# Kernel optimization log

Measured on AMD Instinct MI355X. Metric: run time of the kernel, lower is better.

Reference implementation:

```python
import jax, jax.numpy as jnp
import numpy as np

EPS = 1e-6


def setup_inputs() -> dict:
    key = jax.random.key(0)
    k1, k2, k3, k4 = jax.random.split(key, 4)
    N, H, D = 262144, 256, 64  # total tokens, pc_hidden, cross_att_dim
    return {
        "yhat_embedding": jax.random.normal(k1, (N, H), dtype=jnp.float32),
        "y_embedding": jax.random.normal(k2, (N, H), dtype=jnp.float32),
        "k": jax.random.normal(k3, (H, D), dtype=jnp.float32),
        "q": jax.random.normal(k4, (H, D), dtype=jnp.float32),
        "seg_len": 64,  # uniform scope length (ragged scopes regularized)
    }


def reference(yhat_embedding, y_embedding, k, q, seg_len):
    # Project once for all tokens, then batch the per-segment attention.
    N, H = y_embedding.shape
    D = k.shape[1]
    B = N // seg_len
    yk = (y_embedding @ k).reshape(B, seg_len, D)       # y @ k per segment
    yq = (yhat_embedding @ q).reshape(B, seg_len, D)    # (q.T @ yhat.T).T
    scale = 1.0 / np.sqrt(D).astype(np.float32)
    # M[b] = (1/sqrt(D)) * (y@k) @ (yhat@q).T : [B, L, L]
    M = scale * jnp.einsum("bld,bmd->blm", yk, yq)
    attn = jax.nn.softmax(M, axis=2) + EPS               # softmax over dim=1 of [L,L]
    W = attn / attn.sum(axis=1, keepdims=True)           # column-normalize (axis=0 per segment)
    return W  # [B, L, L] stack of per-scope cross matrices
```

## Files before the change

### kernel.cpp

```cpp
#include <hip/hip_runtime.h>


#define H  256
#define D  64
#define L  64

typedef __attribute__((ext_vector_type(8))) short frag_b;
typedef __attribute__((ext_vector_type(4))) float frag_acc;

__device__ inline unsigned short f32_bf16_rne(float f) {
    unsigned u = __float_as_uint(f);
    u += 0x7FFFu + ((u >> 16) & 1u);
    return (unsigned short)(u >> 16);
}
__device__ inline float bf16_f32(unsigned short h) {
    return __uint_as_float(((unsigned)h) << 16);
}

__device__ inline int pswz(int row, int col) {
    return (row << 6) + ((((col >> 3) ^ row) & 7) << 3) + (col & 7);
}

__global__ void prep_kq(const float* __restrict__ k, const float* __restrict__ q,
                        unsigned short* __restrict__ planes) {
    int tid = blockIdx.x * 256 + threadIdx.x;
    const float* src = (tid < H * D) ? k : q;
    int base = (tid < H * D) ? 0 : 2 * H * D;
    int e = tid & (H * D - 1);
    int h = e >> 6, d = e & 63;
    float x = src[e];
    unsigned short hi = f32_bf16_rne(x);
    float rem = x - bf16_f32(hi);
    unsigned short lo = f32_bf16_rne(rem);
    int o = d * H + h;
    planes[base + o] = hi;
    planes[base + H * D + o] = lo;
}

__global__ __launch_bounds__(256, 5) void cross_attn(
        const float* __restrict__ yhat, const float* __restrict__ y,
        const unsigned short* __restrict__ planes, float* __restrict__ out) {
    __shared__ __align__(16) unsigned short s_pl[4 * L * D];

    const int b    = blockIdx.x;
    const int tid  = threadIdx.x;
    const int wave = tid >> 6;
    const int lane = tid & 63;
    const int ln   = lane & 15;
    const int kg   = lane >> 4;

    const bool isQ = (wave >= 2);
    const float* src = isQ ? yhat : y;
    const frag_b* bph = (const frag_b*)(planes + (isQ ? 2 * H * D : 0));
    const frag_b* bpl = bph + (H * D) / 8;
    const int rowbase = (wave & 1) * 32;

    const frag_acc zf = {0.f, 0.f, 0.f, 0.f};
    frag_acc acc[2][4];
    #pragma unroll
    for (int rt = 0; rt < 2; rt++)
        #pragma unroll
        for (int t = 0; t < 4; t++) acc[rt][t] = zf;

    const float* abase = src + ((size_t)b * L + rowbase + ln) * H + kg * 8;

    #pragma unroll 2
    for (int ks = 0; ks < 8; ks++) {
        const int kb = ks * 32;
        float4 v[2][2];
        #pragma unroll
        for (int rt = 0; rt < 2; rt++) {
            const float4* ap = (const float4*)(abase + (size_t)rt * 16 * H + kb);
            v[rt][0] = ap[0];
            v[rt][1] = ap[1];
        }
        frag_b ah[2], al[2];
        #pragma unroll
        for (int rt = 0; rt < 2; rt++) {
            float xs[8] = {v[rt][0].x, v[rt][0].y, v[rt][0].z, v[rt][0].w,
                           v[rt][1].x, v[rt][1].y, v[rt][1].z, v[rt][1].w};
            #pragma unroll
            for (int j = 0; j < 8; j++) {
                unsigned short hb = f32_bf16_rne(xs[j]);
                ah[rt][j] = (short)hb;
                al[rt][j] = (short)f32_bf16_rne(xs[j] - bf16_f32(hb));
            }
        }
        #pragma unroll
        for (int t = 0; t < 4; t++) {
            int n = t * 16 + ln;
            frag_b bh = bph[n * (H / 8) + ks * 4 + kg];
            frag_b bl = bpl[n * (H / 8) + ks * 4 + kg];
            #pragma unroll
            for (int rt = 0; rt < 2; rt++) {
                acc[rt][t] = __builtin_amdgcn_mfma_f32_16x16x32_bf16(ah[rt], bh, acc[rt][t], 0, 0, 0);
                acc[rt][t] = __builtin_amdgcn_mfma_f32_16x16x32_bf16(ah[rt], bl, acc[rt][t], 0, 0, 0);
                acc[rt][t] = __builtin_amdgcn_mfma_f32_16x16x32_bf16(al[rt], bh, acc[rt][t], 0, 0, 0);
            }
        }
    }

    {
        unsigned short* dstH = s_pl + (isQ ? 2 * L * D : 0);
        unsigned short* dstL = dstH + L * D;
        #pragma unroll
        for (int rt = 0; rt < 2; rt++)
            #pragma unroll
            for (int t = 0; t < 4; t++)
                #pragma unroll
                for (int i = 0; i < 4; i++) {
                    int row = rowbase + rt * 16 + kg * 4 + i;
                    int col = t * 16 + ln;
                    float x = acc[rt][t][i];
                    unsigned short hb = f32_bf16_rne(x);
                    int o = pswz(row, col);
                    dstH[o] = hb;
                    dstL[o] = f32_bf16_rne(x - bf16_f32(hb));
                }
    }
    __syncthreads();

    const unsigned short* ykH = s_pl;
    const unsigned short* ykL = s_pl + L * D;
    const unsigned short* yqH = s_pl + 2 * L * D;
    const unsigned short* yqL = s_pl + 3 * L * D;

    frag_acc mac[4];
    #pragma unroll
    for (int t = 0; t < 4; t++) mac[t] = zf;

    #pragma unroll
    for (int dk = 0; dk < 2; dk++) {
        const int colb = dk * 32 + kg * 8;
        frag_b ah = *(const frag_b*)(ykH + pswz(wave * 16 + ln, colb));
        frag_b al = *(const frag_b*)(ykL + pswz(wave * 16 + ln, colb));
        #pragma unroll
        for (int t = 0; t < 4; t++) {
            frag_b bh = *(const frag_b*)(yqH + pswz(t * 16 + ln, colb));
            frag_b bl = *(const frag_b*)(yqL + pswz(t * 16 + ln, colb));
            mac[t] = __builtin_amdgcn_mfma_f32_16x16x32_bf16(ah, bh, mac[t], 0, 0, 0);
            mac[t] = __builtin_amdgcn_mfma_f32_16x16x32_bf16(ah, bl, mac[t], 0, 0, 0);
            mac[t] = __builtin_amdgcn_mfma_f32_16x16x32_bf16(al, bh, mac[t], 0, 0, 0);
        }
    }
    __syncthreads();

    float* s_cs = (float*)s_pl;

    float a[4][4];
    float colpart[4] = {0.f, 0.f, 0.f, 0.f};
    #pragma unroll
    for (int i = 0; i < 4; i++) {
        float v0 = 0.125f * mac[0][i], v1 = 0.125f * mac[1][i];
        float v2 = 0.125f * mac[2][i], v3 = 0.125f * mac[3][i];
        float mx = fmaxf(fmaxf(v0, v1), fmaxf(v2, v3));
        #pragma unroll
        for (int off = 8; off >= 1; off >>= 1) mx = fmaxf(mx, __shfl_xor(mx, off, 64));
        float e0 = __expf(v0 - mx), e1 = __expf(v1 - mx);
        float e2 = __expf(v2 - mx), e3 = __expf(v3 - mx);
        float s = (e0 + e1) + (e2 + e3);
        #pragma unroll
        for (int off = 8; off >= 1; off >>= 1) s += __shfl_xor(s, off, 64);
        float rs = 1.f / s;
        a[0][i] = e0 * rs + 1e-6f; a[1][i] = e1 * rs + 1e-6f;
        a[2][i] = e2 * rs + 1e-6f; a[3][i] = e3 * rs + 1e-6f;
        colpart[0] += a[0][i]; colpart[1] += a[1][i];
        colpart[2] += a[2][i]; colpart[3] += a[3][i];
    }
    #pragma unroll
    for (int t = 0; t < 4; t++) {
        colpart[t] += __shfl_xor(colpart[t], 16, 64);
        colpart[t] += __shfl_xor(colpart[t], 32, 64);
    }
    s_cs[wave * 64 + kg * 16 + ln] = colpart[kg];
    __syncthreads();

    float* ob = out + (size_t)b * (L * L);
    #pragma unroll
    for (int t = 0; t < 4; t++) {
        int c = t * 16 + ln;
        float inv = 1.f / (s_cs[c] + s_cs[64 + c] + s_cs[128 + c] + s_cs[192 + c]);
        #pragma unroll
        for (int i = 0; i < 4; i++)
            ob[(wave * 16 + kg * 4 + i) * 64 + c] = a[t][i] * inv;
    }
}

extern "C" void kernel_launch(void* const* d_in, const int* in_sizes, int n_in,
                              void* d_out, int out_size, void* d_ws, size_t ws_size,
                              hipStream_t stream) {
    const float* yhat = (const float*)d_in[0];
    const float* y    = (const float*)d_in[1];
    const float* k    = (const float*)d_in[2];
    const float* q    = (const float*)d_in[3];
    float* outp = (float*)d_out;
    unsigned short* planes = (unsigned short*)d_ws;

    const int N = in_sizes[0] / H;
    const int B = N / L;

    prep_kq<<<(2 * H * D) / 256, 256, 0, stream>>>(k, q, planes);
    cross_attn<<<B, 256, 0, stream>>>(yhat, y, planes, outp);
}
```

Measured before the change: 604.0 us.

## Split fused cross-attention into separate projection and mixing kernels via workspace

Splits the kernel in two. A projection kernel computes y@k and yhat@q over 128-row tiles, with B fragments loaded ahead of the MFMAs, and writes swizzled bf16 hi/lo planes to the workspace. A second mixing kernel loads those planes into shared memory and runs the L×L product, softmax and column normalisation. The aim is to give the projection GEMM its own launch shape and occupancy, where before two waves per matrix did it inside a per-segment block. The cost is an extra global round trip of about 512 bytes per token. The old fused kernel stays as a fallback when the workspace is too small.

```diff
diff --git a/kernel.cpp b/kernel.cpp
--- a/kernel.cpp
+++ b/kernel.cpp
@@ -37,9 +37,88 @@
     planes[base + H * D + o] = lo;
 }
 
-__global__ __launch_bounds__(256, 5) void cross_attn(
-        const float* __restrict__ yhat, const float* __restrict__ y,
-        const unsigned short* __restrict__ planes, float* __restrict__ out) {
+__global__ __launch_bounds__(256, 4) void proj(
+        const float* __restrict__ y, const float* __restrict__ yhat,
+        const unsigned short* __restrict__ kq, unsigned short* __restrict__ pl2) {
+    const int mat  = blockIdx.y;
+    const float* src = mat ? yhat : y;
+    const frag_b* bph = (const frag_b*)(kq + mat * 2 * H * D);
+    const frag_b* bpl = bph + (H * D) / 8;
+    const int tid  = threadIdx.x;
+    const int wave = tid >> 6;
+    const int lane = tid & 63;
+    const int ln   = lane & 15;
+    const int kg   = lane >> 4;
+    const int row0 = blockIdx.x * 128 + wave * 32;
+
+    const frag_acc zf = {0.f, 0.f, 0.f, 0.f};
+    frag_acc acc[2][4];
+    #pragma unroll
+    for (int rt = 0; rt < 2; rt++)
+        #pragma unroll
+        for (int t = 0; t < 4; t++) acc[rt][t] = zf;
+
+    const float* abase = src + ((size_t)(row0 + ln)) * H + kg * 8;
+
+    #pragma unroll 2
+    for (int ks = 0; ks < 8; ks++) {
+        const int kb = ks * 32;
+        float4 v[2][2];
+        #pragma unroll
+        for (int rt = 0; rt < 2; rt++) {
+            const float4* ap = (const float4*)(abase + (size_t)rt * 16 * H + kb);
+            v[rt][0] = ap[0];
+            v[rt][1] = ap[1];
+        }
+        frag_b bh[4], bl[4];
+        #pragma unroll
+        for (int t = 0; t < 4; t++) {
+            int n = t * 16 + ln;
+            bh[t] = bph[n * (H / 8) + ks * 4 + kg];
+            bl[t] = bpl[n * (H / 8) + ks * 4 + kg];
+        }
+        frag_b ah[2], al[2];
+        #pragma unroll
+        for (int rt = 0; rt < 2; rt++) {
+            float xs[8] = {v[rt][0].x, v[rt][0].y, v[rt][0].z, v[rt][0].w,
+                           v[rt][1].x, v[rt][1].y, v[rt][1].z, v[rt][1].w};
+            #pragma unroll
+            for (int j = 0; j < 8; j++) {
+                unsigned short hb = f32_bf16_rne(xs[j]);
+                ah[rt][j] = (short)hb;
+                al[rt][j] = (short)f32_bf16_rne(xs[j] - bf16_f32(hb));
+            }
+        }
+        #pragma unroll
+        for (int t = 0; t < 4; t++)
+            #pragma unroll
+            for (int rt = 0; rt < 2; rt++) {
+                acc[rt][t] = __builtin_amdgcn_mfma_f32_16x16x32_bf16(ah[rt], bh[t], acc[rt][t], 0, 0, 0);
+                acc[rt][t] = __builtin_amdgcn_mfma_f32_16x16x32_bf16(ah[rt], bl[t], acc[rt][t], 0, 0, 0);
+                acc[rt][t] = __builtin_amdgcn_mfma_f32_16x16x32_bf16(al[rt], bh[t], acc[rt][t], 0, 0, 0);
+            }
+    }
+
+    #pragma unroll
+    for (int rt = 0; rt < 2; rt++)
+        #pragma unroll
+        for (int t = 0; t < 4; t++)
+            #pragma unroll
+            for (int i = 0; i < 4; i++) {
+                int rg  = row0 + rt * 16 + kg * 4 + i;
+                int seg = rg >> 6, r = rg & 63;
+                int col = t * 16 + ln;
+                int o   = pswz(r, col);
+                unsigned short* mb = pl2 + (size_t)seg * 16384 + mat * 8192;
+                float x = acc[rt][t][i];
+                unsigned short hb = f32_bf16_rne(x);
+                mb[o]        = hb;
+                mb[4096 + o] = f32_bf16_rne(x - bf16_f32(hb));
+            }
+}
+
+__global__ __launch_bounds__(256, 5) void mix(
+        const unsigned short* __restrict__ pl2, float* __restrict__ out) {
     __shared__ __align__(16) unsigned short s_pl[4 * L * D];
 
     const int b    = blockIdx.x;
@@ -49,6 +128,93 @@
     const int ln   = lane & 15;
     const int kg   = lane >> 4;
 
+    {
+        const float4* g4 = (const float4*)(pl2 + (size_t)b * 16384);
+        float4* s4 = (float4*)s_pl;
+        #pragma unroll
+        for (int i = 0; i < 8; i++) s4[i * 256 + tid] = g4[i * 256 + tid];
+    }
+    __syncthreads();
+
+    const unsigned short* ykH = s_pl;
+    const unsigned short* ykL = s_pl + L * D;
+    const unsigned short* yqH = s_pl + 2 * L * D;
+    const unsigned short* yqL = s_pl + 3 * L * D;
+
+    const frag_acc zf = {0.f, 0.f, 0.f, 0.f};
+    frag_acc mac[4];
+    #pragma unroll
+    for (int t = 0; t < 4; t++) mac[t] = zf;
+
+    #pragma unroll
+    for (int dk = 0; dk < 2; dk++) {
+        const int colb = dk * 32 + kg * 8;
+        frag_b ah = *(const frag_b*)(ykH + pswz(wave * 16 + ln, colb));
+        frag_b al = *(const frag_b*)(ykL + pswz(wave * 16 + ln, colb));
+        #pragma unroll
+        for (int t = 0; t < 4; t++) {
+            frag_b bh = *(const frag_b*)(yqH + pswz(t * 16 + ln, colb));
+            frag_b bl = *(const frag_b*)(yqL + pswz(t * 16 + ln, colb));
+            mac[t] = __builtin_amdgcn_mfma_f32_16x16x32_bf16(ah, bh, mac[t], 0, 0, 0);
+            mac[t] = __builtin_amdgcn_mfma_f32_16x16x32_bf16(ah, bl, mac[t], 0, 0, 0);
+            mac[t] = __builtin_amdgcn_mfma_f32_16x16x32_bf16(al, bh, mac[t], 0, 0, 0);
+        }
+    }
+    __syncthreads();
+
+    float* s_cs = (float*)s_pl;
+
+    float a[4][4];
+    float colpart[4] = {0.f, 0.f, 0.f, 0.f};
+    #pragma unroll
+    for (int i = 0; i < 4; i++) {
+        float v0 = 0.125f * mac[0][i], v1 = 0.125f * mac[1][i];
+        float v2 = 0.125f * mac[2][i], v3 = 0.125f * mac[3][i];
+        float mx = fmaxf(fmaxf(v0, v1), fmaxf(v2, v3));
+        #pragma unroll
+        for (int off = 8; off >= 1; off >>= 1) mx = fmaxf(mx, __shfl_xor(mx, off, 64));
+        float e0 = __expf(v0 - mx), e1 = __expf(v1 - mx);
+        float e2 = __expf(v2 - mx), e3 = __expf(v3 - mx);
+        float s = (e0 + e1) + (e2 + e3);
+        #pragma unroll
+        for (int off = 8; off >= 1; off >>= 1) s += __shfl_xor(s, off, 64);
+        float rs = 1.f / s;
+        a[0][i] = e0 * rs + 1e-6f; a[1][i] = e1 * rs + 1e-6f;
+        a[2][i] = e2 * rs + 1e-6f; a[3][i] = e3 * rs + 1e-6f;
+        colpart[0] += a[0][i]; colpart[1] += a[1][i];
+        colpart[2] += a[2][i]; colpart[3] += a[3][i];
+    }
+    #pragma unroll
+    for (int t = 0; t < 4; t++) {
+        colpart[t] += __shfl_xor(colpart[t], 16, 64);
+        colpart[t] += __shfl_xor(colpart[t], 32, 64);
+    }
+    s_cs[wave * 64 + kg * 16 + ln] = colpart[kg];
+    __syncthreads();
+
+    float* ob = out + (size_t)b * (L * L);
+    #pragma unroll
+    for (int t = 0; t < 4; t++) {
+        int c = t * 16 + ln;
+        float inv = 1.f / (s_cs[c] + s_cs[64 + c] + s_cs[128 + c] + s_cs[192 + c]);
+        #pragma unroll
+        for (int i = 0; i < 4; i++)
+            ob[(wave * 16 + kg * 4 + i) * 64 + c] = a[t][i] * inv;
+    }
+}
+
+__global__ __launch_bounds__(256, 5) void cross_attn_fused(
+        const float* __restrict__ yhat, const float* __restrict__ y,
+        const unsigned short* __restrict__ planes, float* __restrict__ out) {
+    __shared__ __align__(16) unsigned short s_pl[4 * L * D];
+
+    const int b    = blockIdx.x;
+    const int tid  = threadIdx.x;
+    const int wave = tid >> 6;
+    const int lane = tid & 63;
+    const int ln   = lane & 15;
+    const int kg   = lane >> 4;
+
     const bool isQ = (wave >= 2);
     const float* src = isQ ? yhat : y;
     const frag_b* bph = (const frag_b*)(planes + (isQ ? 2 * H * D : 0));
@@ -99,7 +265,6 @@
             }
         }
     }
-
     {
         unsigned short* dstH = s_pl + (isQ ? 2 * L * D : 0);
         unsigned short* dstL = dstH + L * D;
@@ -146,7 +311,6 @@
     __syncthreads();
 
     float* s_cs = (float*)s_pl;
-
     float a[4][4];
     float colpart[4] = {0.f, 0.f, 0.f, 0.f};
     #pragma unroll
@@ -200,5 +364,13 @@
     const int B = N / L;
 
     prep_kq<<<(2 * H * D) / 256, 256, 0, stream>>>(k, q, planes);
-    cross_attn<<<B, 256, 0, stream>>>(yhat, y, planes, outp);
-}
+
+    const size_t need = 128 * 1024 + (size_t)N * 512;
+    if (ws_size >= need) {
+        unsigned short* pl2 = (unsigned short*)((char*)d_ws + 128 * 1024);
+        proj<<<dim3(N / 128, 2), 256, 0, stream>>>(y, yhat, planes, pl2);
+        mix<<<B, 256, 0, stream>>>(pl2, outp);
+    } else {
+        cross_attn_fused<<<B, 256, 0, stream>>>(yhat, y, planes, outp);
+    }
+}
```

After: 650.3 us. 7.7% more time.

## Stage activation tiles through swizzled LDS with prefetch and relayout k/q fragments

Applied to the files above, without the earlier changes.

Each block now cooperatively loads the 64x256 y and yhat rows with coalesced float4 reads into a swizzled 64 KB LDS buffer. It processes two 32-row halves, prefetching the second half into registers while the first is computed. The k/q bf16 hi/lo planes are rearranged so each lane's MFMA B fragments are contiguous. This is meant to replace strided per-lane global reads with coalesced traffic, at the cost of lower occupancy (2 blocks/CU) and extra barriers.

```diff
diff --git a/kernel.cpp b/kernel.cpp
--- a/kernel.cpp
+++ b/kernel.cpp
@@ -22,25 +22,59 @@
 }
 
 __global__ void prep_kq(const float* __restrict__ k, const float* __restrict__ q,
-                        unsigned short* __restrict__ planes) {
+                        unsigned short* __restrict__ kqF) {
     int tid = blockIdx.x * 256 + threadIdx.x;
-    const float* src = (tid < H * D) ? k : q;
-    int base = (tid < H * D) ? 0 : 2 * H * D;
+    int m   = (tid >= H * D) ? 1 : 0;
+    const float* src = m ? q : k;
     int e = tid & (H * D - 1);
     int h = e >> 6, d = e & 63;
     float x = src[e];
     unsigned short hi = f32_bf16_rne(x);
-    float rem = x - bf16_f32(hi);
-    unsigned short lo = f32_bf16_rne(rem);
-    int o = d * H + h;
-    planes[base + o] = hi;
-    planes[base + H * D + o] = lo;
-}
-
-__global__ __launch_bounds__(256, 5) void cross_attn(
+    unsigned short lo = f32_bf16_rne(x - bf16_f32(hi));
+    int ks = h >> 5, kg = (h >> 3) & 3, j = h & 7;
+    int base = m * 32768 + ks * 2048 + kg * 512 + d * 8 + j;
+    kqF[base]         = hi;
+    kqF[base + 16384] = lo;
+}
+
+__device__ inline void compute_phase(const float* __restrict__ Abuf,
+                                     const frag_b* __restrict__ fbh,
+                                     const frag_b* __restrict__ fbl,
+                                     int rsel, int ln, int kg, frag_acc acc[4]) {
+    const frag_acc zf = {0.f, 0.f, 0.f, 0.f};
+    #pragma unroll
+    for (int t = 0; t < 4; t++) acc[t] = zf;
+    const int rr = rsel + ln;
+    const int s  = rr & 7;
+    const float* rowp = Abuf + rr * 256;
+    #pragma unroll
+    for (int ks = 0; ks < 8; ks++) {
+        const int c0 = ks * 8 + kg * 2;
+        float4 ua = *(const float4*)(rowp + ((c0 ^ s) * 4));
+        float4 ub = *(const float4*)(rowp + (((c0 + 1) ^ s) * 4));
+        float xs[8] = {ua.x, ua.y, ua.z, ua.w, ub.x, ub.y, ub.z, ub.w};
+        frag_b ah, al;
+        #pragma unroll
+        for (int j = 0; j < 8; j++) {
+            unsigned short hb = f32_bf16_rne(xs[j]);
+            ah[j] = (short)hb;
+            al[j] = (short)f32_bf16_rne(xs[j] - bf16_f32(hb));
+        }
+        #pragma unroll
+        for (int t = 0; t < 4; t++) {
+            frag_b bh = fbh[(ks * 4 + kg) * 64 + t * 16 + ln];
+            frag_b bl = fbl[(ks * 4 + kg) * 64 + t * 16 + ln];
+            acc[t] = __builtin_amdgcn_mfma_f32_16x16x32_bf16(ah, bh, acc[t], 0, 0, 0);
+            acc[t] = __builtin_amdgcn_mfma_f32_16x16x32_bf16(ah, bl, acc[t], 0, 0, 0);
+            acc[t] = __builtin_amdgcn_mfma_f32_16x16x32_bf16(al, bh, acc[t], 0, 0, 0);
+        }
+    }
+}
+
+__global__ __launch_bounds__(256, 2) void catt(
         const float* __restrict__ yhat, const float* __restrict__ y,
-        const unsigned short* __restrict__ planes, float* __restrict__ out) {
-    __shared__ __align__(16) unsigned short s_pl[4 * L * D];
+        const unsigned short* __restrict__ kqF, float* __restrict__ out) {
+    __shared__ __align__(16) float lds_f[16384];
 
     const int b    = blockIdx.x;
     const int tid  = threadIdx.x;
@@ -48,83 +82,80 @@
     const int lane = tid & 63;
     const int ln   = lane & 15;
     const int kg   = lane >> 4;
-
-    const bool isQ = (wave >= 2);
-    const float* src = isQ ? yhat : y;
-    const frag_b* bph = (const frag_b*)(planes + (isQ ? 2 * H * D : 0));
-    const frag_b* bpl = bph + (H * D) / 8;
-    const int rowbase = (wave & 1) * 32;
-
-    const frag_acc zf = {0.f, 0.f, 0.f, 0.f};
-    frag_acc acc[2][4];
-    #pragma unroll
-    for (int rt = 0; rt < 2; rt++)
-        #pragma unroll
-        for (int t = 0; t < 4; t++) acc[rt][t] = zf;
-
-    const float* abase = src + ((size_t)b * L + rowbase + ln) * H + kg * 8;
-
-    #pragma unroll 2
-    for (int ks = 0; ks < 8; ks++) {
-        const int kb = ks * 32;
-        float4 v[2][2];
-        #pragma unroll
-        for (int rt = 0; rt < 2; rt++) {
-            const float4* ap = (const float4*)(abase + (size_t)rt * 16 * H + kb);
-            v[rt][0] = ap[0];
-            v[rt][1] = ap[1];
-        }
-        frag_b ah[2], al[2];
-        #pragma unroll
-        for (int rt = 0; rt < 2; rt++) {
-            float xs[8] = {v[rt][0].x, v[rt][0].y, v[rt][0].z, v[rt][0].w,
-                           v[rt][1].x, v[rt][1].y, v[rt][1].z, v[rt][1].w};
-            #pragma unroll
-            for (int j = 0; j < 8; j++) {
-                unsigned short hb = f32_bf16_rne(xs[j]);
-                ah[rt][j] = (short)hb;
-                al[rt][j] = (short)f32_bf16_rne(xs[j] - bf16_f32(hb));
-            }
-        }
-        #pragma unroll
-        for (int t = 0; t < 4; t++) {
-            int n = t * 16 + ln;
-            frag_b bh = bph[n * (H / 8) + ks * 4 + kg];
-            frag_b bl = bpl[n * (H / 8) + ks * 4 + kg];
-            #pragma unroll
-            for (int rt = 0; rt < 2; rt++) {
-                acc[rt][t] = __builtin_amdgcn_mfma_f32_16x16x32_bf16(ah[rt], bh, acc[rt][t], 0, 0, 0);
-                acc[rt][t] = __builtin_amdgcn_mfma_f32_16x16x32_bf16(ah[rt], bl, acc[rt][t], 0, 0, 0);
-                acc[rt][t] = __builtin_amdgcn_mfma_f32_16x16x32_bf16(al[rt], bh, acc[rt][t], 0, 0, 0);
-            }
-        }
-    }
+    const int m    = wave >> 1;
+    const int rsel = (wave & 1) * 16;
+
+    const frag_b* fb  = (const frag_b*)kqF;
+    const frag_b* fbh = fb + (m * 2 + 0) * 2048;
+    const frag_b* fbl = fb + (m * 2 + 1) * 2048;
+
+    const int srow = tid >> 3;
+    const int sq   = tid & 7;
+    const int sswz = srow & 7;
+    const float* rpY0 = y    + ((size_t)(b * 64 + srow)) * 256;
+    const float* rpQ0 = yhat + ((size_t)(b * 64 + srow)) * 256;
+
+    float4 pf[2][8];
+    #pragma unroll
+    for (int i = 0; i < 8; i++) {
+        pf[0][i] = *(const float4*)(rpY0 + (((sq + 8 * i) ^ sswz) * 4));
+        pf[1][i] = *(const float4*)(rpQ0 + (((sq + 8 * i) ^ sswz) * 4));
+    }
+    #pragma unroll
+    for (int i = 0; i < 8; i++) {
+        *(float4*)(lds_f +        srow * 256 + (sq + 8 * i) * 4) = pf[0][i];
+        *(float4*)(lds_f + 8192 + srow * 256 + (sq + 8 * i) * 4) = pf[1][i];
+    }
+    #pragma unroll
+    for (int i = 0; i < 8; i++) {
+        pf[0][i] = *(const float4*)(rpY0 + 32 * 256 + (((sq + 8 * i) ^ sswz) * 4));
+        pf[1][i] = *(const float4*)(rpQ0 + 32 * 256 + (((sq + 8 * i) ^ sswz) * 4));
+    }
+    __syncthreads();
+
+    frag_acc acc0[4];
+    compute_phase(lds_f + m * 8192, fbh, fbl, rsel, ln, kg, acc0);
+    __syncthreads();
+
+    #pragma unroll
+    for (int i = 0; i < 8; i++) {
+        *(float4*)(lds_f +        srow * 256 + (sq + 8 * i) * 4) = pf[0][i];
+        *(float4*)(lds_f + 8192 + srow * 256 + (sq + 8 * i) * 4) = pf[1][i];
+    }
+    __syncthreads();
+
+    frag_acc acc1[4];
+    compute_phase(lds_f + m * 8192, fbh, fbl, rsel, ln, kg, acc1);
+    __syncthreads();
 
     {
-        unsigned short* dstH = s_pl + (isQ ? 2 * L * D : 0);
-        unsigned short* dstL = dstH + L * D;
-        #pragma unroll
-        for (int rt = 0; rt < 2; rt++)
+        unsigned short* img = (unsigned short*)lds_f;
+        unsigned short* mbH = img + m * 8192;
+        unsigned short* mbL = mbH + 4096;
+        #pragma unroll
+        for (int p = 0; p < 2; p++) {
             #pragma unroll
             for (int t = 0; t < 4; t++)
                 #pragma unroll
                 for (int i = 0; i < 4; i++) {
-                    int row = rowbase + rt * 16 + kg * 4 + i;
-                    int col = t * 16 + ln;
-                    float x = acc[rt][t][i];
+                    int r = p * 32 + rsel + kg * 4 + i;
+                    int c = t * 16 + ln;
+                    float x = p ? acc1[t][i] : acc0[t][i];
                     unsigned short hb = f32_bf16_rne(x);
-                    int o = pswz(row, col);
-                    dstH[o] = hb;
-                    dstL[o] = f32_bf16_rne(x - bf16_f32(hb));
+                    int o = pswz(r, c);
+                    mbH[o] = hb;
+                    mbL[o] = f32_bf16_rne(x - bf16_f32(hb));
                 }
-    }
-    __syncthreads();
-
-    const unsigned short* ykH = s_pl;
-    const unsigned short* ykL = s_pl + L * D;
-    const unsigned short* yqH = s_pl + 2 * L * D;
-    const unsigned short* yqL = s_pl + 3 * L * D;
-
+        }
+    }
+    __syncthreads();
+
+    const unsigned short* ykH = (const unsigned short*)lds_f;
+    const unsigned short* ykL = ykH + 4096;
+    const unsigned short* yqH = ykH + 8192;
+    const unsigned short* yqL = ykH + 12288;
+
+    const frag_acc zf = {0.f, 0.f, 0.f, 0.f};
     frag_acc mac[4];
     #pragma unroll
     for (int t = 0; t < 4; t++) mac[t] = zf;
@@ -145,7 +176,7 @@
     }
     __syncthreads();
 
-    float* s_cs = (float*)s_pl;
+    float* s_cs = lds_f + 8192;
 
     float a[4][4];
     float colpart[4] = {0.f, 0.f, 0.f, 0.f};
@@ -194,11 +225,11 @@
     const float* k    = (const float*)d_in[2];
     const float* q    = (const float*)d_in[3];
     float* outp = (float*)d_out;
-    unsigned short* planes = (unsigned short*)d_ws;
+    unsigned short* kqF = (unsigned short*)d_ws;
 
     const int N = in_sizes[0] / H;
     const int B = N / L;
 
-    prep_kq<<<(2 * H * D) / 256, 256, 0, stream>>>(k, q, planes);
-    cross_attn<<<B, 256, 0, stream>>>(yhat, y, planes, outp);
-}
+    prep_kq<<<(2 * H * D) / 256, 256, 0, stream>>>(k, q, kqF);
+    catt<<<B, 256, 0, stream>>>(yhat, y, kqF, outp);
+}
```

Result: slower. 675.2 us (+11.8%).
